# Optimization experiments

Hardware: AMD Instinct MI355X
Metric: run time of the kernel (lower is better)

The kernel has to match this reference:

```python
import jax, jax.numpy as jnp
import numpy as np

N_NODES = 50000
N_EDGES = 800000
IN_F, HID, OUT_F = 128, 128, 64


def setup_inputs() -> dict:
    key = jax.random.key(0)
    k1, k2, k3, k4 = jax.random.split(key, 4)
    x = jax.random.normal(k1, (N_NODES, IN_F), dtype=jnp.float32)
    edge_index = jax.random.randint(k2, (2, N_EDGES), 0, N_NODES, dtype=jnp.int64)
    # Glorot-style scaled weights, zero bias (PyG GCNConv default)
    W1 = jax.random.normal(k3, (IN_F, HID), dtype=jnp.float32) * (1.0 / np.sqrt(IN_F))
    b1 = jnp.zeros((HID,), dtype=jnp.float32)
    W2 = jax.random.normal(k4, (HID, OUT_F), dtype=jnp.float32) * (1.0 / np.sqrt(HID))
    b2 = jnp.zeros((OUT_F,), dtype=jnp.float32)
    return {"x": x, "edge_index": edge_index, "W1": W1, "b1": b1, "W2": W2, "b2": b2}


def reference(x, edge_index, W1, b1, W2, b2):
    n = x.shape[0]
    # add self-loops (PyG GCNConv default add_self_loops=True)
    loop = jnp.arange(n, dtype=edge_index.dtype)
    src = jnp.concatenate([edge_index[0], loop])  # message source nodes
    dst = jnp.concatenate([edge_index[1], loop])  # aggregation target nodes
    # symmetric normalization: D^{-1/2} (A+I) D^{-1/2}
    deg = jax.ops.segment_sum(jnp.ones(dst.shape, dtype=x.dtype), dst, num_segments=n)
    dinv = jnp.where(deg > 0, jax.lax.rsqrt(deg), 0.0)
    norm = dinv[src] * dinv[dst]  # [E+N]

    def gcn_conv(h, W, b):
        h = h @ W                              # dense transform first (PyG order)
        msg = h[src] * norm[:, None]           # gather + scale: [E+N, d]
        agg = jax.ops.segment_sum(msg, dst, num_segments=n)  # scatter-add
        return agg + b

    h = jax.nn.relu(gcn_conv(x, W1, b1))
    return gcn_conv(h, W2, b2)
```

## Files before the change

### kernel.cpp

```cpp
#include <hip/hip_runtime.h>
#include <hip/hip_bf16.h>

#define NN   50000
#define NE   800000
#define F_IN 128
#define F_H  128
#define F_O  64

#define BINSHIFT 7
#define NBINS    ((NN + 127) >> 7)
#define CAP      2816
#define EPB      2048

static constexpr int NB_G1  = (NN + 63) / 64;
static constexpr int NB_BIN = (NE + EPB - 1) / EPB;

typedef __bf16 bf16_8 __attribute__((ext_vector_type(8)));
typedef float  f32x4  __attribute__((ext_vector_type(4)));

template <typename AT, int K, int NOUT, bool SCALE>
__device__ __forceinline__ void gemm_body(const AT* __restrict__ X,
                                          const float* __restrict__ W,
                                          const float* __restrict__ dinv,
                                          __hip_bfloat16* __restrict__ Y,
                                          __hip_bfloat16* WB, int blk) {
    constexpr int NKS = K / 32;
    constexpr int NC  = NOUT / 16;
    const int t = threadIdx.x;
    for (int f = t; f < K * NOUT; f += 256) {
        int k = f / NOUT, n = f % NOUT;
        int ks = k >> 5, kr = k & 31, qq = kr >> 3, jj = kr & 7;
        int c = n >> 4, nn = n & 15;
        WB[(((ks * NC + c) * 16 + nn) * 4 + qq) * 8 + jj] = __float2bfloat16(W[f]);
    }
    __syncthreads();

    const int wave = t >> 6, lane = t & 63;
    const int r = lane & 15, q = lane >> 4;
    const int m0 = blk * 64 + wave * 16;
    int arow = m0 + r;
    if (arow >= NN) arow = NN - 1;

    f32x4 acc[NC];
#pragma unroll
    for (int c = 0; c < NC; ++c) acc[c] = (f32x4){0.f, 0.f, 0.f, 0.f};

#pragma unroll
    for (int ks = 0; ks < NKS; ++ks) {
        bf16_8 a;
        if constexpr (sizeof(AT) == 4) {
            const float* xp = (const float*)X + (size_t)arow * K + ks * 32 + q * 8;
            float4 x0 = ((const float4*)xp)[0];
            float4 x1 = ((const float4*)xp)[1];
            a[0] = (__bf16)x0.x; a[1] = (__bf16)x0.y; a[2] = (__bf16)x0.z; a[3] = (__bf16)x0.w;
            a[4] = (__bf16)x1.x; a[5] = (__bf16)x1.y; a[6] = (__bf16)x1.z; a[7] = (__bf16)x1.w;
        } else {
            a = *(const bf16_8*)((const __hip_bfloat16*)X + (size_t)arow * K + ks * 32 + q * 8);
        }
#pragma unroll
        for (int c = 0; c < NC; ++c) {
            bf16_8 b = *(const bf16_8*)&WB[(((ks * NC + c) * 16 + r) * 4 + q) * 8];
            acc[c] = __builtin_amdgcn_mfma_f32_16x16x32_bf16(a, b, acc[c], 0, 0, 0);
        }
    }

#pragma unroll
    for (int c = 0; c < NC; ++c) {
#pragma unroll
        for (int i = 0; i < 4; ++i) {
            int gr = m0 + q * 4 + i;
            if (gr < NN) {
                float v = acc[c][i];
                if constexpr (SCALE) v *= dinv[gr];
                Y[(size_t)gr * NOUT + c * 16 + r] = __float2bfloat16(v);
            }
        }
    }
}

__global__ __launch_bounds__(256) void k_fuseA(const float* __restrict__ X,
                                               const float* __restrict__ W1,
                                               __hip_bfloat16* __restrict__ Xw,
                                               const int* __restrict__ ei32,
                                               int* __restrict__ binbuf,
                                               unsigned* __restrict__ bincnt) {
    __shared__ __align__(16) char smem[32768];
    const int t = threadIdx.x;

    if (blockIdx.x >= NB_BIN) {
        gemm_body<float, F_IN, F_H, false>(X, W1, nullptr, Xw,
                                           (__hip_bfloat16*)smem,
                                           blockIdx.x - NB_BIN);
        return;
    }

    unsigned* hist = (unsigned*)smem;
    unsigned* base = hist + NBINS;
    unsigned* rank = base + NBINS;
    for (int i = t; i < NBINS; i += 256) { hist[i] = 0u; rank[i] = 0u; }
    __syncthreads();

    const bool is64 = ((ei32[1] | ei32[3] | ei32[5] | ei32[7]) == 0);
    const int e0 = blockIdx.x * EPB;
    int pk[8], bin[8];
#pragma unroll
    for (int j = 0; j < 8; ++j) {
        int e = e0 + t + j * 256;
        if (e < NE) {
            int s, d;
            if (is64) {
                const long long* p = (const long long*)ei32;
                s = (int)p[e];
                d = (int)p[NE + e];
            } else {
                s = ei32[e];
                d = ei32[NE + e];
            }
            pk[j]  = (s << BINSHIFT) | (d & 127);
            bin[j] = d >> BINSHIFT;
        } else bin[j] = -1;
    }
#pragma unroll
    for (int j = 0; j < 8; ++j)
        if (bin[j] >= 0) atomicAdd(&hist[bin[j]], 1u);
    __syncthreads();
    for (int b = t; b < NBINS; b += 256)
        base[b] = atomicAdd(&bincnt[b], hist[b]);
    __syncthreads();
#pragma unroll
    for (int j = 0; j < 8; ++j) {
        if (bin[j] >= 0) {
            unsigned rk = atomicAdd(&rank[bin[j]], 1u);
            binbuf[(size_t)bin[j] * CAP + base[bin[j]] + rk] = pk[j];
        }
    }
}

__global__ __launch_bounds__(256) void k_phaseB(const int* __restrict__ binbuf,
                                                const unsigned* __restrict__ bincnt,
                                                unsigned* __restrict__ row_ptr,
                                                float* __restrict__ dinv,
                                                int* __restrict__ srcs) {
    __shared__ unsigned h[128];
    __shared__ unsigned cur[128];
    __shared__ unsigned red[256];
    const int b = blockIdx.x, t = threadIdx.x;

    unsigned part = 0;
    for (int i = t; i < NBINS; i += 256)
        if (i < b) part += bincnt[i];
    red[t] = part;
    if (t < 128) h[t] = 0u;
    __syncthreads();
    for (int off = 128; off > 0; off >>= 1) {
        if (t < off) red[t] += red[t + off];
        __syncthreads();
    }
    const unsigned gbase = red[0];

    const unsigned n = bincnt[b];
    const int* buf = binbuf + (size_t)b * CAP;
    for (unsigned i = t; i < n; i += 256)
        atomicAdd(&h[buf[i] & 127], 1u);
    __syncthreads();
    if (t < 128) cur[t] = h[t];
    __syncthreads();
    for (int off = 1; off < 128; off <<= 1) {
        unsigned u = (t < 128 && t >= off) ? cur[t - off] : 0u;
        __syncthreads();
        if (t < 128) cur[t] += u;
        __syncthreads();
    }
    if (t < 128) {
        unsigned ex = gbase + cur[t] - h[t];
        int node = (b << BINSHIFT) + t;
        if (node < NN) {
            row_ptr[node] = ex;
            dinv[node]    = rsqrtf((float)(h[t] + 1u));
        }
        cur[t] = ex;
    }
    if (b == NBINS - 1 && t == 0) row_ptr[NN] = NE;
    __syncthreads();
    for (unsigned i = t; i < n; i += 256) {
        int p = buf[i];
        unsigned pos = atomicAdd(&cur[p & 127], 1u);
        srcs[pos] = p >> BINSHIFT;
    }
}

__global__ __launch_bounds__(256) void k_agg1(const __hip_bfloat16* __restrict__ Xw,
                                              const int* __restrict__ srcs,
                                              const unsigned* __restrict__ row_ptr,
                                              const float* __restrict__ dinv,
                                              const float* __restrict__ b1,
                                              __hip_bfloat16* __restrict__ H) {
    const int wv   = (blockIdx.x * 256 + threadIdx.x) >> 6;
    const int lane = threadIdx.x & 63;
    if (wv >= NN) return;
    const int sub = lane >> 4;
    const int fl  = lane & 15;
    const float dn = dinv[wv];

    float acc0[8], acc1[8];
    bf16_8 self = *(const bf16_8*)(Xw + (size_t)wv * F_H + fl * 8);
    const float sw = (sub == 0) ? dn : 0.f;
#pragma unroll
    for (int j = 0; j < 8; ++j) { acc0[j] = sw * (float)self[j]; acc1[j] = 0.f; }

    const unsigned ie = row_ptr[wv + 1];
    unsigned i = row_ptr[wv] + sub;
    for (; i + 4 < ie; i += 8) {
        int s0 = srcs[i], s1 = srcs[i + 4];
        float d0 = dinv[s0], d1 = dinv[s1];
        bf16_8 r0 = *(const bf16_8*)(Xw + (size_t)s0 * F_H + fl * 8);
        bf16_8 r1 = *(const bf16_8*)(Xw + (size_t)s1 * F_H + fl * 8);
#pragma unroll
        for (int j = 0; j < 8; ++j) {
            acc0[j] += d0 * (float)r0[j];
            acc1[j] += d1 * (float)r1[j];
        }
    }
    if (i < ie) {
        int s = srcs[i];
        float d = dinv[s];
        bf16_8 r = *(const bf16_8*)(Xw + (size_t)s * F_H + fl * 8);
#pragma unroll
        for (int j = 0; j < 8; ++j) acc0[j] += d * (float)r[j];
    }
#pragma unroll
    for (int j = 0; j < 8; ++j) {
        float a = acc0[j] + acc1[j];
        a += __shfl_xor(a, 16, 64);
        a += __shfl_xor(a, 32, 64);
        acc0[j] = a;
    }
    if (sub == 0) {
        bf16_8 o;
#pragma unroll
        for (int j = 0; j < 8; ++j) {
            float v = fmaxf(dn * acc0[j] + b1[fl * 8 + j], 0.f);
            o[j] = (__bf16)v;
        }
        *(bf16_8*)(H + (size_t)wv * F_H + fl * 8) = o;
    }
}

__global__ __launch_bounds__(256) void k_gemm2(const __hip_bfloat16* __restrict__ H1,
                                               const float* __restrict__ W2,
                                               const float* __restrict__ dinv,
                                               __hip_bfloat16* __restrict__ Hw) {
    __shared__ __align__(16) __hip_bfloat16 WB[(F_H / 32) * (F_O / 16) * 512];
    gemm_body<__hip_bfloat16, F_H, F_O, true>(H1, W2, dinv, Hw, WB, blockIdx.x);
}

__global__ __launch_bounds__(256) void k_agg2(const __hip_bfloat16* __restrict__ Hw,
                                              const int* __restrict__ srcs,
                                              const unsigned* __restrict__ row_ptr,
                                              const float* __restrict__ dinv,
                                              const float* __restrict__ b2,
                                              float* __restrict__ out) {
    const int wv   = (blockIdx.x * 256 + threadIdx.x) >> 6;
    const int lane = threadIdx.x & 63;
    if (wv >= NN) return;
    const int sub = lane >> 3;
    const int fl  = lane & 7;

    float acc0[8], acc1[8];
    bf16_8 self = *(const bf16_8*)(Hw + (size_t)wv * F_O + fl * 8);
#pragma unroll
    for (int j = 0; j < 8; ++j) {
        acc0[j] = (sub == 0) ? (float)self[j] : 0.f;
        acc1[j] = 0.f;
    }

    const unsigned ie = row_ptr[wv + 1];
    unsigned i = row_ptr[wv] + sub;
    for (; i + 8 < ie; i += 16) {
        int s0 = srcs[i], s1 = srcs[i + 8];
        bf16_8 r0 = *(const bf16_8*)(Hw + (size_t)s0 * F_O + fl * 8);
        bf16_8 r1 = *(const bf16_8*)(Hw + (size_t)s1 * F_O + fl * 8);
#pragma unroll
        for (int j = 0; j < 8; ++j) {
            acc0[j] += (float)r0[j];
            acc1[j] += (float)r1[j];
        }
    }
    if (i < ie) {
        int s = srcs[i];
        bf16_8 r = *(const bf16_8*)(Hw + (size_t)s * F_O + fl * 8);
#pragma unroll
        for (int j = 0; j < 8; ++j) acc0[j] += (float)r[j];
    }
#pragma unroll
    for (int j = 0; j < 8; ++j) {
        float a = acc0[j] + acc1[j];
        a += __shfl_xor(a, 8, 64);
        a += __shfl_xor(a, 16, 64);
        a += __shfl_xor(a, 32, 64);
        acc0[j] = a;
    }
    if (sub == 0) {
        float dn = dinv[wv];
        float4 o0 = make_float4(dn * acc0[0] + b2[fl * 8 + 0], dn * acc0[1] + b2[fl * 8 + 1],
                                dn * acc0[2] + b2[fl * 8 + 2], dn * acc0[3] + b2[fl * 8 + 3]);
        float4 o1 = make_float4(dn * acc0[4] + b2[fl * 8 + 4], dn * acc0[5] + b2[fl * 8 + 5],
                                dn * acc0[6] + b2[fl * 8 + 6], dn * acc0[7] + b2[fl * 8 + 7]);
        float4* op = (float4*)(out + (size_t)wv * F_O + fl * 8);
        op[0] = o0;
        op[1] = o1;
    }
}

extern "C" void kernel_launch(void* const* d_in, const int* in_sizes, int n_in,
                              void* d_out, int out_size, void* d_ws, size_t ws_size,
                              hipStream_t stream) {
    const float* x  = (const float*)d_in[0];
    const int*   ei = (const int*)d_in[1];
    const float* W1 = (const float*)d_in[2];
    const float* b1 = (const float*)d_in[3];
    const float* W2 = (const float*)d_in[4];
    const float* b2 = (const float*)d_in[5];
    float* out = (float*)d_out;

    char* w = (char*)d_ws;
    size_t off = 0;
    auto alloc = [&](size_t bytes) {
        void* p = w + off;
        off += (bytes + 255) & ~(size_t)255;
        return p;
    };
    unsigned* row_ptr = (unsigned*)alloc((size_t)(NN + 1) * 4);
    float*    dinv    = (float*)alloc((size_t)NN * 4);
    unsigned* bincnt  = (unsigned*)alloc((size_t)NBINS * 4);
    int*      srcs    = (int*)alloc((size_t)NE * 4);
    int*      binbuf  = (int*)alloc((size_t)NBINS * CAP * 4);
    __hip_bfloat16* Xw = (__hip_bfloat16*)alloc((size_t)NN * F_H * 2);
    __hip_bfloat16* H1 = (__hip_bfloat16*)alloc((size_t)NN * F_H * 2);
    __hip_bfloat16* Hw = Xw;

    hipMemsetAsync(bincnt, 0, (size_t)NBINS * 4, stream);
    k_fuseA<<<NB_BIN + NB_G1, 256, 0, stream>>>(x, W1, Xw, ei, binbuf, bincnt);
    k_phaseB<<<NBINS, 256, 0, stream>>>(binbuf, bincnt, row_ptr, dinv, srcs);

    k_agg1<<<(NN + 3) / 4, 256, 0, stream>>>(Xw, srcs, row_ptr, dinv, b1, H1);
    k_gemm2<<<(NN + 63) / 64, 256, 0, stream>>>(H1, W2, dinv, Hw);
    k_agg2<<<(NN + 3) / 4, 256, 0, stream>>>(Hw, srcs, row_ptr, dinv, b2, out);
}
```

Before: 192.1 us.

## Fuse CSR build, layer-1 aggregation and second GEMM into one per-bin kernel

```diff
diff --git a/kernel.cpp b/kernel.cpp
--- a/kernel.cpp
+++ b/kernel.cpp
@@ -11,6 +11,7 @@
 #define NBINS    ((NN + 127) >> 7)
 #define CAP      2816
 #define EPB      2048
+#define RPSTRIDE 132
 
 static constexpr int NB_G1  = (NN + 63) / 64;
 static constexpr int NB_BIN = (NE + EPB - 1) / EPB;
@@ -18,10 +19,9 @@
 typedef __bf16 bf16_8 __attribute__((ext_vector_type(8)));
 typedef float  f32x4  __attribute__((ext_vector_type(4)));
 
-template <typename AT, int K, int NOUT, bool SCALE>
+template <typename AT, int K, int NOUT>
 __device__ __forceinline__ void gemm_body(const AT* __restrict__ X,
                                           const float* __restrict__ W,
-                                          const float* __restrict__ dinv,
                                           __hip_bfloat16* __restrict__ Y,
                                           __hip_bfloat16* WB, int blk) {
     constexpr int NKS = K / 32;
@@ -69,11 +69,8 @@
 #pragma unroll
         for (int i = 0; i < 4; ++i) {
             int gr = m0 + q * 4 + i;
-            if (gr < NN) {
-                float v = acc[c][i];
-                if constexpr (SCALE) v *= dinv[gr];
-                Y[(size_t)gr * NOUT + c * 16 + r] = __float2bfloat16(v);
-            }
+            if (gr < NN)
+                Y[(size_t)gr * NOUT + c * 16 + r] = __float2bfloat16(acc[c][i]);
         }
     }
 }
@@ -83,14 +80,14 @@
                                                __hip_bfloat16* __restrict__ Xw,
                                                const int* __restrict__ ei32,
                                                int* __restrict__ binbuf,
-                                               unsigned* __restrict__ bincnt) {
+                                               unsigned* __restrict__ bincnt,
+                                               unsigned* __restrict__ cnt) {
     __shared__ __align__(16) char smem[32768];
     const int t = threadIdx.x;
 
     if (blockIdx.x >= NB_BIN) {
-        gemm_body<float, F_IN, F_H, false>(X, W1, nullptr, Xw,
-                                           (__hip_bfloat16*)smem,
-                                           blockIdx.x - NB_BIN);
+        gemm_body<float, F_IN, F_H>(X, W1, Xw, (__hip_bfloat16*)smem,
+                                    blockIdx.x - NB_BIN);
         return;
     }
 
@@ -102,7 +99,7 @@
 
     const bool is64 = ((ei32[1] | ei32[3] | ei32[5] | ei32[7]) == 0);
     const int e0 = blockIdx.x * EPB;
-    int pk[8], bin[8];
+    int pk[8], bin[8], dd[8];
 #pragma unroll
     for (int j = 0; j < 8; ++j) {
         int e = e0 + t + j * 256;
@@ -118,11 +115,16 @@
             }
             pk[j]  = (s << BINSHIFT) | (d & 127);
             bin[j] = d >> BINSHIFT;
+            dd[j]  = d;
         } else bin[j] = -1;
     }
 #pragma unroll
-    for (int j = 0; j < 8; ++j)
-        if (bin[j] >= 0) atomicAdd(&hist[bin[j]], 1u);
+    for (int j = 0; j < 8; ++j) {
+        if (bin[j] >= 0) {
+            atomicAdd(&hist[bin[j]], 1u);
+            atomicAdd(&cnt[dd[j]], 1u);
+        }
+    }
     __syncthreads();
     for (int b = t; b < NBINS; b += 256)
         base[b] = atomicAdd(&bincnt[b], hist[b]);
@@ -136,31 +138,38 @@
     }
 }
 
-__global__ __launch_bounds__(256) void k_phaseB(const int* __restrict__ binbuf,
-                                                const unsigned* __restrict__ bincnt,
-                                                unsigned* __restrict__ row_ptr,
-                                                float* __restrict__ dinv,
-                                                int* __restrict__ srcs) {
-    __shared__ unsigned h[128];
-    __shared__ unsigned cur[128];
-    __shared__ unsigned red[256];
+#define HS 136
+__global__ __launch_bounds__(1024) void k_phaseC(const int* __restrict__ binbuf,
+                                                 const unsigned* __restrict__ bincnt,
+                                                 const unsigned* __restrict__ cnt,
+                                                 const __hip_bfloat16* __restrict__ Xw,
+                                                 const float* __restrict__ W2,
+                                                 const float* __restrict__ b1,
+                                                 __hip_bfloat16* __restrict__ Hw,
+                                                 int* __restrict__ srcs_g,
+                                                 unsigned short* __restrict__ rp_g) {
+    __shared__ __align__(16) char smem[64000];
+    __hip_bfloat16* Htile = (__hip_bfloat16*)smem;
+    __hip_bfloat16* WB2   = (__hip_bfloat16*)(smem + 34816);
+    int*      srcsL = (int*)(smem + 34816 + 16384);
+    unsigned* h     = (unsigned*)(smem + 62464);
+    unsigned* cur   = (unsigned*)(smem + 62976);
+    float*    dv    = (float*)(smem + 63488);
+
     const int b = blockIdx.x, t = threadIdx.x;
 
-    unsigned part = 0;
-    for (int i = t; i < NBINS; i += 256)
-        if (i < b) part += bincnt[i];
-    red[t] = part;
+    for (int f = t; f < F_H * F_O; f += 1024) {
+        int k = f / F_O, n = f % F_O;
+        int ks = k >> 5, kr = k & 31, qq = kr >> 3, jj = kr & 7;
+        int c = n >> 4, nn = n & 15;
+        WB2[(((ks * 4 + c) * 16 + nn) * 4 + qq) * 8 + jj] = __float2bfloat16(W2[f]);
+    }
     if (t < 128) h[t] = 0u;
     __syncthreads();
-    for (int off = 128; off > 0; off >>= 1) {
-        if (t < off) red[t] += red[t + off];
-        __syncthreads();
-    }
-    const unsigned gbase = red[0];
 
     const unsigned n = bincnt[b];
     const int* buf = binbuf + (size_t)b * CAP;
-    for (unsigned i = t; i < n; i += 256)
+    for (unsigned i = t; i < n; i += 1024)
         atomicAdd(&h[buf[i] & 127], 1u);
     __syncthreads();
     if (t < 128) cur[t] = h[t];
@@ -172,99 +181,119 @@
         __syncthreads();
     }
     if (t < 128) {
-        unsigned ex = gbase + cur[t] - h[t];
-        int node = (b << BINSHIFT) + t;
-        if (node < NN) {
-            row_ptr[node] = ex;
-            dinv[node]    = rsqrtf((float)(h[t] + 1u));
-        }
+        unsigned ex = cur[t] - h[t];
+        rp_g[b * RPSTRIDE + t] = (unsigned short)ex;
+        if (t == 0) rp_g[b * RPSTRIDE + 128] = (unsigned short)n;
+        dv[t]  = rsqrtf((float)(h[t] + 1u));
         cur[t] = ex;
     }
-    if (b == NBINS - 1 && t == 0) row_ptr[NN] = NE;
-    __syncthreads();
-    for (unsigned i = t; i < n; i += 256) {
+    __syncthreads();
+    for (unsigned i = t; i < n; i += 1024) {
         int p = buf[i];
         unsigned pos = atomicAdd(&cur[p & 127], 1u);
-        srcs[pos] = p >> BINSHIFT;
-    }
-}
-
-__global__ __launch_bounds__(256) void k_agg1(const __hip_bfloat16* __restrict__ Xw,
-                                              const int* __restrict__ srcs,
-                                              const unsigned* __restrict__ row_ptr,
-                                              const float* __restrict__ dinv,
-                                              const float* __restrict__ b1,
-                                              __hip_bfloat16* __restrict__ H) {
-    const int wv   = (blockIdx.x * 256 + threadIdx.x) >> 6;
-    const int lane = threadIdx.x & 63;
-    if (wv >= NN) return;
-    const int sub = lane >> 4;
-    const int fl  = lane & 15;
-    const float dn = dinv[wv];
-
-    float acc0[8], acc1[8];
-    bf16_8 self = *(const bf16_8*)(Xw + (size_t)wv * F_H + fl * 8);
-    const float sw = (sub == 0) ? dn : 0.f;
-#pragma unroll
-    for (int j = 0; j < 8; ++j) { acc0[j] = sw * (float)self[j]; acc1[j] = 0.f; }
-
-    const unsigned ie = row_ptr[wv + 1];
-    unsigned i = row_ptr[wv] + sub;
-    for (; i + 4 < ie; i += 8) {
-        int s0 = srcs[i], s1 = srcs[i + 4];
-        float d0 = dinv[s0], d1 = dinv[s1];
-        bf16_8 r0 = *(const bf16_8*)(Xw + (size_t)s0 * F_H + fl * 8);
-        bf16_8 r1 = *(const bf16_8*)(Xw + (size_t)s1 * F_H + fl * 8);
+        int s = p >> BINSHIFT;
+        srcsL[pos] = s;
+        srcs_g[(size_t)b * CAP + pos] = s;
+    }
+    __syncthreads();
+
+    const int wave = t >> 6, lane = t & 63;
+    const int fl = lane & 15, sub = lane >> 4;
+    const float4 b1a = ((const float4*)b1)[fl * 2];
+    const float4 b1b = ((const float4*)b1)[fl * 2 + 1];
+    for (int nd = 0; nd < 8; ++nd) {
+        const int tl    = wave * 8 + nd;
+        const int gnode = (b << BINSHIFT) + tl;
+        const unsigned i1 = cur[tl];
+        const unsigned i0 = i1 - h[tl];
+        float acc0[8], acc1[8];
+        {
+            int sv = (gnode < NN) ? gnode : 0;
+            bf16_8 r = *(const bf16_8*)(Xw + (size_t)sv * F_H + fl * 8);
+            float w = (sub == 0 && gnode < NN) ? dv[tl] : 0.f;
+#pragma unroll
+            for (int j = 0; j < 8; ++j) { acc0[j] = w * (float)r[j]; acc1[j] = 0.f; }
+        }
+        unsigned i = i0 + sub;
+        for (; i + 4 < i1; i += 8) {
+            int s0 = srcsL[i], s1 = srcsL[i + 4];
+            float w0 = rsqrtf((float)(cnt[s0] + 1u));
+            float w1 = rsqrtf((float)(cnt[s1] + 1u));
+            bf16_8 r0 = *(const bf16_8*)(Xw + (size_t)s0 * F_H + fl * 8);
+            bf16_8 r1 = *(const bf16_8*)(Xw + (size_t)s1 * F_H + fl * 8);
+#pragma unroll
+            for (int j = 0; j < 8; ++j) {
+                acc0[j] += w0 * (float)r0[j];
+                acc1[j] += w1 * (float)r1[j];
+            }
+        }
+        if (i < i1) {
+            int s = srcsL[i];
+            float w = rsqrtf((float)(cnt[s] + 1u));
+            bf16_8 r = *(const bf16_8*)(Xw + (size_t)s * F_H + fl * 8);
+#pragma unroll
+            for (int j = 0; j < 8; ++j) acc0[j] += w * (float)r[j];
+        }
 #pragma unroll
         for (int j = 0; j < 8; ++j) {
-            acc0[j] += d0 * (float)r0[j];
-            acc1[j] += d1 * (float)r1[j];
-        }
-    }
-    if (i < ie) {
-        int s = srcs[i];
-        float d = dinv[s];
-        bf16_8 r = *(const bf16_8*)(Xw + (size_t)s * F_H + fl * 8);
-#pragma unroll
-        for (int j = 0; j < 8; ++j) acc0[j] += d * (float)r[j];
-    }
-#pragma unroll
-    for (int j = 0; j < 8; ++j) {
-        float a = acc0[j] + acc1[j];
-        a += __shfl_xor(a, 16, 64);
-        a += __shfl_xor(a, 32, 64);
-        acc0[j] = a;
-    }
-    if (sub == 0) {
-        bf16_8 o;
-#pragma unroll
-        for (int j = 0; j < 8; ++j) {
-            float v = fmaxf(dn * acc0[j] + b1[fl * 8 + j], 0.f);
-            o[j] = (__bf16)v;
-        }
-        *(bf16_8*)(H + (size_t)wv * F_H + fl * 8) = o;
-    }
-}
-
-__global__ __launch_bounds__(256) void k_gemm2(const __hip_bfloat16* __restrict__ H1,
-                                               const float* __restrict__ W2,
-                                               const float* __restrict__ dinv,
-                                               __hip_bfloat16* __restrict__ Hw) {
-    __shared__ __align__(16) __hip_bfloat16 WB[(F_H / 32) * (F_O / 16) * 512];
-    gemm_body<__hip_bfloat16, F_H, F_O, true>(H1, W2, dinv, Hw, WB, blockIdx.x);
+            float a = acc0[j] + acc1[j];
+            a += __shfl_xor(a, 16, 64);
+            a += __shfl_xor(a, 32, 64);
+            acc0[j] = a;
+        }
+        if (sub == 0) {
+            const float bias[8] = {b1a.x, b1a.y, b1a.z, b1a.w, b1b.x, b1b.y, b1b.z, b1b.w};
+            bf16_8 o;
+#pragma unroll
+            for (int j = 0; j < 8; ++j)
+                o[j] = (__bf16)fmaxf(dv[tl] * acc0[j] + bias[j], 0.f);
+            *(bf16_8*)(Htile + tl * HS + fl * 8) = o;
+        }
+    }
+    __syncthreads();
+
+    {
+        const int r = lane & 15, q = lane >> 4;
+        const int rt = wave >> 1;
+        const int c0 = (wave & 1) * 2;
+        f32x4 acc[2] = {(f32x4){0.f, 0.f, 0.f, 0.f}, (f32x4){0.f, 0.f, 0.f, 0.f}};
+#pragma unroll
+        for (int ks = 0; ks < 4; ++ks) {
+            bf16_8 a = *(const bf16_8*)(Htile + (rt * 16 + r) * HS + ks * 32 + q * 8);
+#pragma unroll
+            for (int cc = 0; cc < 2; ++cc) {
+                bf16_8 bb = *(const bf16_8*)&WB2[(((ks * 4 + (c0 + cc)) * 16 + r) * 4 + q) * 8];
+                acc[cc] = __builtin_amdgcn_mfma_f32_16x16x32_bf16(a, bb, acc[cc], 0, 0, 0);
+            }
+        }
+#pragma unroll
+        for (int cc = 0; cc < 2; ++cc) {
+#pragma unroll
+            for (int i = 0; i < 4; ++i) {
+                int tl = rt * 16 + q * 4 + i;
+                int gnode = (b << BINSHIFT) + tl;
+                if (gnode < NN)
+                    Hw[(size_t)gnode * F_O + (c0 + cc) * 16 + r] =
+                        __float2bfloat16(dv[tl] * acc[cc][i]);
+            }
+        }
+    }
 }
 
 __global__ __launch_bounds__(256) void k_agg2(const __hip_bfloat16* __restrict__ Hw,
-                                              const int* __restrict__ srcs,
-                                              const unsigned* __restrict__ row_ptr,
-                                              const float* __restrict__ dinv,
+                                              const int* __restrict__ srcs_g,
+                                              const unsigned short* __restrict__ rp_g,
                                               const float* __restrict__ b2,
                                               float* __restrict__ out) {
     const int wv   = (blockIdx.x * 256 + threadIdx.x) >> 6;
     const int lane = threadIdx.x & 63;
     if (wv >= NN) return;
+    const int bin = wv >> BINSHIFT, tl = wv & 127;
     const int sub = lane >> 3;
     const int fl  = lane & 7;
+    const unsigned i0 = rp_g[bin * RPSTRIDE + tl];
+    const unsigned i1 = rp_g[bin * RPSTRIDE + tl + 1];
+    const int* srcs = srcs_g + (size_t)bin * CAP;
 
     float acc0[8], acc1[8];
     bf16_8 self = *(const bf16_8*)(Hw + (size_t)wv * F_O + fl * 8);
@@ -274,9 +303,8 @@
         acc1[j] = 0.f;
     }
 
-    const unsigned ie = row_ptr[wv + 1];
-    unsigned i = row_ptr[wv] + sub;
-    for (; i + 8 < ie; i += 16) {
+    unsigned i = i0 + sub;
+    for (; i + 8 < i1; i += 16) {
         int s0 = srcs[i], s1 = srcs[i + 8];
         bf16_8 r0 = *(const bf16_8*)(Hw + (size_t)s0 * F_O + fl * 8);
         bf16_8 r1 = *(const bf16_8*)(Hw + (size_t)s1 * F_O + fl * 8);
@@ -286,7 +314,7 @@
             acc1[j] += (float)r1[j];
         }
     }
-    if (i < ie) {
+    if (i < i1) {
         int s = srcs[i];
         bf16_8 r = *(const bf16_8*)(Hw + (size_t)s * F_O + fl * 8);
 #pragma unroll
@@ -301,7 +329,7 @@
         acc0[j] = a;
     }
     if (sub == 0) {
-        float dn = dinv[wv];
+        float dn = rsqrtf((float)(i1 - i0 + 1u));
         float4 o0 = make_float4(dn * acc0[0] + b2[fl * 8 + 0], dn * acc0[1] + b2[fl * 8 + 1],
                                 dn * acc0[2] + b2[fl * 8 + 2], dn * acc0[3] + b2[fl * 8 + 3]);
         float4 o1 = make_float4(dn * acc0[4] + b2[fl * 8 + 4], dn * acc0[5] + b2[fl * 8 + 5],
@@ -330,20 +358,18 @@
         off += (bytes + 255) & ~(size_t)255;
         return p;
     };
-    unsigned* row_ptr = (unsigned*)alloc((size_t)(NN + 1) * 4);
-    float*    dinv    = (float*)alloc((size_t)NN * 4);
+    unsigned* cnt     = (unsigned*)alloc((size_t)NN * 4);
     unsigned* bincnt  = (unsigned*)alloc((size_t)NBINS * 4);
-    int*      srcs    = (int*)alloc((size_t)NE * 4);
     int*      binbuf  = (int*)alloc((size_t)NBINS * CAP * 4);
+    int*      srcs    = (int*)alloc((size_t)NBINS * CAP * 4);
+    unsigned short* rp = (unsigned short*)alloc((size_t)NBINS * RPSTRIDE * 2);
     __hip_bfloat16* Xw = (__hip_bfloat16*)alloc((size_t)NN * F_H * 2);
-    __hip_bfloat16* H1 = (__hip_bfloat16*)alloc((size_t)NN * F_H * 2);
-    __hip_bfloat16* Hw = Xw;
-
-    hipMemsetAsync(bincnt, 0, (size_t)NBINS * 4, stream);
-    k_fuseA<<<NB_BIN + NB_G1, 256, 0, stream>>>(x, W1, Xw, ei, binbuf, bincnt);
-    k_phaseB<<<NBINS, 256, 0, stream>>>(binbuf, bincnt, row_ptr, dinv, srcs);
-
-    k_agg1<<<(NN + 3) / 4, 256, 0, stream>>>(Xw, srcs, row_ptr, dinv, b1, H1);
-    k_gemm2<<<(NN + 63) / 64, 256, 0, stream>>>(H1, W2, dinv, Hw);
-    k_agg2<<<(NN + 3) / 4, 256, 0, stream>>>(Hw, srcs, row_ptr, dinv, b2, out);
-}
+    __hip_bfloat16* Hw = (__hip_bfloat16*)alloc((size_t)NN * F_O * 2);
+
+    size_t zlen = (((size_t)NN * 4 + 255) & ~(size_t)255) + (size_t)NBINS * 4;
+    hipMemsetAsync(cnt, 0, zlen, stream);
+
+    k_fuseA<<<NB_BIN + NB_G1, 256, 0, stream>>>(x, W1, Xw, ei, binbuf, bincnt, cnt);
+    k_phaseC<<<NBINS, 1024, 0, stream>>>(binbuf, bincnt, cnt, Xw, W2, b1, Hw, srcs, rp);
+    k_agg2<<<(NN + 3) / 4, 256, 0, stream>>>(Hw, srcs, rp, b2, out);
+}
```

Result: slower. 199.4 us (+3.8%).

## Bin more edges per block with a two-pass loop and re-layout GEMM weight tile

Applied to the files above, without the earlier changes.

```diff
diff --git a/kernel.cpp b/kernel.cpp
--- a/kernel.cpp
+++ b/kernel.cpp
@@ -10,10 +10,11 @@
 #define BINSHIFT 7
 #define NBINS    ((NN + 127) >> 7)
 #define CAP      2816
-#define EPB      2048
+#define EPB      8192
 
 static constexpr int NB_G1  = (NN + 63) / 64;
 static constexpr int NB_BIN = (NE + EPB - 1) / EPB;
+static constexpr int NB_NODE = (NN + 255) / 256;
 
 typedef __bf16 bf16_8 __attribute__((ext_vector_type(8)));
 typedef float  f32x4  __attribute__((ext_vector_type(4)));
@@ -31,7 +32,7 @@
         int k = f / NOUT, n = f % NOUT;
         int ks = k >> 5, kr = k & 31, qq = kr >> 3, jj = kr & 7;
         int c = n >> 4, nn = n & 15;
-        WB[(((ks * NC + c) * 16 + nn) * 4 + qq) * 8 + jj] = __float2bfloat16(W[f]);
+        WB[(((ks * NC + c) * 4 + qq) * 16 + nn) * 8 + jj] = __float2bfloat16(W[f]);
     }
     __syncthreads();
 
@@ -59,7 +60,7 @@
         }
 #pragma unroll
         for (int c = 0; c < NC; ++c) {
-            bf16_8 b = *(const bf16_8*)&WB[(((ks * NC + c) * 16 + r) * 4 + q) * 8];
+            bf16_8 b = *(const bf16_8*)&WB[(((ks * NC + c) * 4 + q) * 16 + r) * 8];
             acc[c] = __builtin_amdgcn_mfma_f32_16x16x32_bf16(a, b, acc[c], 0, 0, 0);
         }
     }
@@ -101,38 +102,25 @@
     __syncthreads();
 
     const bool is64 = ((ei32[1] | ei32[3] | ei32[5] | ei32[7]) == 0);
+    const long long* p64 = (const long long*)ei32;
     const int e0 = blockIdx.x * EPB;
-    int pk[8], bin[8];
-#pragma unroll
-    for (int j = 0; j < 8; ++j) {
-        int e = e0 + t + j * 256;
-        if (e < NE) {
-            int s, d;
-            if (is64) {
-                const long long* p = (const long long*)ei32;
-                s = (int)p[e];
-                d = (int)p[NE + e];
-            } else {
-                s = ei32[e];
-                d = ei32[NE + e];
-            }
-            pk[j]  = (s << BINSHIFT) | (d & 127);
-            bin[j] = d >> BINSHIFT;
-        } else bin[j] = -1;
-    }
-#pragma unroll
-    for (int j = 0; j < 8; ++j)
-        if (bin[j] >= 0) atomicAdd(&hist[bin[j]], 1u);
+    const int e1 = (e0 + EPB < NE) ? e0 + EPB : NE;
+
+    for (int e = e0 + t; e < e1; e += 256) {
+        int d = is64 ? (int)p64[NE + e] : ei32[NE + e];
+        atomicAdd(&hist[d >> BINSHIFT], 1u);
+    }
     __syncthreads();
     for (int b = t; b < NBINS; b += 256)
         base[b] = atomicAdd(&bincnt[b], hist[b]);
     __syncthreads();
-#pragma unroll
-    for (int j = 0; j < 8; ++j) {
-        if (bin[j] >= 0) {
-            unsigned rk = atomicAdd(&rank[bin[j]], 1u);
-            binbuf[(size_t)bin[j] * CAP + base[bin[j]] + rk] = pk[j];
-        }
+    for (int e = e0 + t; e < e1; e += 256) {
+        int s, d;
+        if (is64) { s = (int)p64[e]; d = (int)p64[NE + e]; }
+        else      { s = ei32[e];     d = ei32[NE + e]; }
+        int b = d >> BINSHIFT;
+        unsigned rk = atomicAdd(&rank[b], 1u);
+        binbuf[(size_t)b * CAP + base[b] + rk] = (s << BINSHIFT) | (d & 127);
     }
 }
 
```

New measurement: 186.7 us. 2.8% less time.
